# Performance work log

Measured on AMD Instinct MI355X. Metric: run time of the kernel, lower is better.

Reference implementation:

```python
import jax, jax.numpy as jnp
import numpy as np

C, V, B, ITERS = 144, 576, 1024, 3  # checks, variables, batch, decoding iterations
COL_W = 4  # variable-node degree (ones per column of H)


def _make_H():
    """Deterministic sparse 0/1 parity-check matrix, col weight COL_W, row weight >= 2."""
    rng = np.random.default_rng(0)
    H = np.zeros((C, V), np.float32)
    for v in range(V):
        H[rng.choice(C, size=COL_W, replace=False), v] = 1.0
    for c in range(C):
        while H[c].sum() < 2:
            H[c, rng.integers(V)] = 1.0
    return H


def setup_inputs() -> dict:
    key = jax.random.key(0)
    r = jax.random.normal(key, (B, V), dtype=jnp.float32)  # channel LLRs, batched
    alpha = 0.7 * jnp.ones((ITERS,), dtype=jnp.float32)    # nn.Parameter init
    H = jnp.asarray(_make_H())                             # [C, V] 0/1 mask
    return {"r": r, "alpha": alpha, "H": H}


def _c_to_v(M, edge, a):
    """Check-to-variable min-sum messages, vectorized over batch and rows.

    For each edge (c,v): E[c,v] = a * (prod of signs of M[c, edges(c)\\{v}])
                                   * (min of |M[c, edges(c)\\{v}]|)
    Implemented with the standard two-smallest-values trick.
    """
    inf = jnp.float32(jnp.inf)
    absM = jnp.where(edge, jnp.abs(M), inf)                 # [B,C,V]
    min1 = jnp.min(absM, axis=-1, keepdims=True)            # smallest |M| per row
    idx = jnp.argmin(absM, axis=-1)                         # [B,C] its position
    is_min = jnp.arange(V)[None, None, :] == idx[..., None]  # one-hot of argmin
    min2 = jnp.min(jnp.where(is_min, inf, absM), axis=-1, keepdims=True)
    excl_min = jnp.where(is_min, min2, min1)                # min excluding self
    sgn = jnp.where(edge, jnp.sign(M), 1.0)
    row_sign = jnp.prod(sgn, axis=-1, keepdims=True)
    sgn_excl = row_sign * sgn                               # product excluding self (signs are +/-1)
    return jnp.where(edge, a * sgn_excl * excl_min, 0.0)


def reference(r, alpha, H):
    edge = (H == 1.0)[None, :, :]                           # [1,C,V] broadcast to batch
    rB = r[:, None, :]                                      # [B,1,V]
    M = jnp.where(edge, rB, 0.0)                            # initial_M: M[c,v]=r[v] on edges
    E = jnp.zeros_like(M)
    for i in range(alpha.shape[0]):
        E = _c_to_v(M, edge, alpha[i])
        col = jnp.sum(E, axis=1, keepdims=True)             # [B,1,V] sum over checks
        M = jnp.where(edge, col - E + rB, 0.0)              # update_M: extrinsic sum + r[v]
    return r + jnp.sum(E, axis=1)                           # [B,V] output LLRs
```

## Files before the change

kernel.cpp:

```cpp
#include <hip/hip_runtime.h>
#include <stdint.h>

#define CN 144
#define VN 576
#define BN 1024
#define NITER 3
#define RCAP 32
#define NQ   (RCAP/4)
#define CCAP 8
#define TPB 192

#define WS_RLEN 0
#define WS_LOC  192
#define WS_CSC  (192 + CN*VN)
#define WS_CCNT (WS_CSC + CCAP*VN)

__device__ __forceinline__ int edge_id(int l, int c) {
    return (((l >> 2) * CN + c) << 2) | (l & 3);
}

__global__ __launch_bounds__(64) void build_stage(const float* __restrict__ H,
                                                  int* __restrict__ ws) {
    const int c = blockIdx.x;
    const int lane = threadIdx.x;
    int base = 0;
    const float* row = H + c * VN;
    for (int ch = 0; ch < VN / 64; ++ch) {
        const int v = ch * 64 + lane;
        const bool set = row[v] > 0.5f;
        const unsigned long long mask = __ballot(set);
        const int off = base + (int)__popcll(mask & ((1ULL << lane) - 1ULL));
        ws[WS_LOC + v * CN + c] = set ? off : -1;
        base += (int)__popcll(mask);
    }
    if (lane == 0) ws[WS_RLEN + c] = base;
}

__global__ __launch_bounds__(64) void build_csc(int* __restrict__ ws) {
    const int v = blockIdx.x;
    const int lane = threadIdx.x;
    int cnt = 0;
    for (int ch = 0; ch < 3; ++ch) {
        const int c = ch * 64 + lane;
        const int l = (c < CN) ? ws[WS_LOC + v * CN + c] : -1;
        const bool set = (l >= 0) && (l < RCAP);
        const unsigned long long mask = __ballot(set);
        const int off = cnt + (int)__popcll(mask & ((1ULL << lane) - 1ULL));
        if (set && off < CCAP) ws[WS_CSC + off * VN + v] = edge_id(l, c);
        cnt += (int)__popcll(mask);
    }
    if (cnt > CCAP) cnt = CCAP;
    if (lane == 0) ws[WS_CCNT + v] = cnt;
    if (lane >= cnt && lane < CCAP) ws[WS_CSC + lane * VN + v] = 0;
}

__global__ __launch_bounds__(TPB) void ldpc_decode(const float* __restrict__ r,
                                                   const float* __restrict__ alpha,
                                                   const int* __restrict__ ws,
                                                   float* __restrict__ out) {
    __shared__ float4 M4[NQ * CN];
    float* const Mf = reinterpret_cast<float*>(M4);

    const int b = blockIdx.x;
    const int t = threadIdx.x;
    const float a_[NITER] = { alpha[0], alpha[1], alpha[2] };

    int ent4[3][4], entX[3][4];
    int cnt[3];
    float rv[3];
    #pragma unroll
    for (int q = 0; q < 3; ++q) {
        const int v = t + q * TPB;
        rv[q]  = r[b * VN + v];
        cnt[q] = ws[WS_CCNT + v];
        #pragma unroll
        for (int j = 0; j < 4; ++j) ent4[q][j] = ws[WS_CSC + j * VN + v];
    }
    const int rl = (t < CN) ? min(ws[WS_RLEN + t], RCAP) : 0;
    const int any_hi = __syncthreads_or((cnt[0] > 4) | (cnt[1] > 4) | (cnt[2] > 4));
    if (any_hi) {
        #pragma unroll
        for (int q = 0; q < 3; ++q)
            #pragma unroll
            for (int j = 0; j < 4; ++j) entX[q][j] = ws[WS_CSC + (4 + j) * VN + t + q * TPB];
    }

    if (t < CN) {
        const int rpad = (rl + 3) & ~3;
        for (int k = rl; k < rpad; ++k) Mf[edge_id(k, t)] = INFINITY;
    }
    #pragma unroll
    for (int q = 0; q < 3; ++q) {
        #pragma unroll
        for (int j = 0; j < 4; ++j) if (j < cnt[q]) Mf[ent4[q][j]] = rv[q];
    }
    if (any_hi) {
        #pragma unroll
        for (int q = 0; q < 3; ++q) {
            #pragma unroll
            for (int j = 0; j < 4; ++j) if (4 + j < cnt[q]) Mf[entX[q][j]] = rv[q];
        }
    }
    __syncthreads();

    #pragma unroll
    for (int it = 0; it < NITER; ++it) {
        const float a = a_[it];

        if (t < CN) {
            const int nq  = (rl + 3) >> 2;
            const int nqf = rl >> 2;
            float4 mq[NQ];
            uint32_t m1 = 0x7fffffffu, m2 = 0x7fffffffu, sg = 0u;
            #pragma unroll
            for (int q4 = 0; q4 < NQ; ++q4) {
                if (q4 < nq) {
                    mq[q4] = M4[q4 * CN + t];
                    const uint32_t* mu = reinterpret_cast<const uint32_t*>(&mq[q4]);
                    #pragma unroll
                    for (int j = 0; j < 4; ++j) {
                        const uint32_t mb = mu[j];
                        const uint32_t ab = mb & 0x7fffffffu;
                        sg ^= mb;
                        const uint32_t hi = (ab > m1) ? ab : m1;
                        m1 = (ab < m1) ? ab : m1;
                        m2 = (hi < m2) ? hi : m2;
                    }
                }
            }
            sg &= 0x80000000u;
            const uint32_t p1b = __float_as_uint(a * __uint_as_float(m1)) ^ sg;
            const uint32_t p2b = __float_as_uint(a * __uint_as_float(m2)) ^ sg;
            #pragma unroll
            for (int q4 = 0; q4 < NQ; ++q4) {
                if (q4 < nq) {
                    const uint32_t* mu = reinterpret_cast<const uint32_t*>(&mq[q4]);
                    float4 ev;
                    uint32_t* eu = reinterpret_cast<uint32_t*>(&ev);
                    if (q4 < nqf) {
                        #pragma unroll
                        for (int j = 0; j < 4; ++j) {
                            const uint32_t mb = mu[j];
                            const uint32_t ab = mb & 0x7fffffffu;
                            eu[j] = ((ab == m1) ? p2b : p1b) ^ (mb & 0x80000000u);
                        }
                    } else {
                        #pragma unroll
                        for (int j = 0; j < 4; ++j) {
                            const int k = q4 * 4 + j;
                            const uint32_t mb = mu[j];
                            const uint32_t ab = mb & 0x7fffffffu;
                            eu[j] = (k < rl)
                                  ? (((ab == m1) ? p2b : p1b) ^ (mb & 0x80000000u))
                                  : mb;
                        }
                    }
                    M4[q4 * CN + t] = ev;
                }
            }
        }
        __syncthreads();

        #pragma unroll
        for (int q = 0; q < 3; ++q) {
            float E4[4], EX[4];
            float col = 0.0f;
            #pragma unroll
            for (int j = 0; j < 4; ++j) {
                E4[j] = (j < cnt[q]) ? Mf[ent4[q][j]] : 0.0f;
                col += E4[j];
            }
            if (any_hi) {
                #pragma unroll
                for (int j = 0; j < 4; ++j) {
                    EX[j] = (4 + j < cnt[q]) ? Mf[entX[q][j]] : 0.0f;
                    col += EX[j];
                }
            }
            if (it == NITER - 1) {
                out[b * VN + t + q * TPB] = rv[q] + col;
            } else {
                const float mb = col + rv[q];
                #pragma unroll
                for (int j = 0; j < 4; ++j) if (j < cnt[q]) Mf[ent4[q][j]] = mb - E4[j];
                if (any_hi) {
                    #pragma unroll
                    for (int j = 0; j < 4; ++j) if (4 + j < cnt[q]) Mf[entX[q][j]] = mb - EX[j];
                }
            }
        }
        if (it < NITER - 1) __syncthreads();
    }
}

extern "C" void kernel_launch(void* const* d_in, const int* in_sizes, int n_in,
                              void* d_out, int out_size, void* d_ws, size_t ws_size,
                              hipStream_t stream) {
    const float* r     = (const float*)d_in[0];
    const float* alpha = (const float*)d_in[1];
    const float* H     = (const float*)d_in[2];
    float* out = (float*)d_out;
    int* ws    = (int*)d_ws;

    build_stage<<<CN, 64, 0, stream>>>(H, ws);
    build_csc<<<VN, 64, 0, stream>>>(ws);
    ldpc_decode<<<BN, TPB, 0, stream>>>(r, alpha, ws, out);
}
```

Baseline: 23.73 us.

## Fuse graph-building kernels via atomic row-slot counters and fixed-width row scans

The two preprocessing kernels become one. Each column builder now claims a row slot with an atomicAdd on a per-check counter, taken modulo 32, instead of reading a precomputed dense location table. This removes a kernel launch and the large LOC workspace pass. The decoder drops per-row lengths: it pre-fills shared memory with infinities, scans all 8 float4 slots per row, and passes the infinity entries through unchanged. In exchange it does a little more shared-memory and ALU work per iteration, and the counters are never reset between calls, so correctness depends on row degree staying at or below 32.

New measurement: 25.04 us. 1.06x slower.

```diff
diff --git a/kernel.cpp b/kernel.cpp
--- a/kernel.cpp
+++ b/kernel.cpp
@@ -5,48 +5,32 @@
 #define VN 576
 #define BN 1024
 #define NITER 3
-#define RCAP 32
-#define NQ   (RCAP/4)
+#define NQ   8
 #define CCAP 8
 #define TPB 192
 
-#define WS_RLEN 0
-#define WS_LOC  192
-#define WS_CSC  (192 + CN*VN)
-#define WS_CCNT (WS_CSC + CCAP*VN)
+#define WS_RCTR 0
+#define WS_CCNT 144
+#define WS_CSC  720
 
 __device__ __forceinline__ int edge_id(int l, int c) {
     return (((l >> 2) * CN + c) << 2) | (l & 3);
 }
 
-__global__ __launch_bounds__(64) void build_stage(const float* __restrict__ H,
-                                                  int* __restrict__ ws) {
-    const int c = blockIdx.x;
-    const int lane = threadIdx.x;
-    int base = 0;
-    const float* row = H + c * VN;
-    for (int ch = 0; ch < VN / 64; ++ch) {
-        const int v = ch * 64 + lane;
-        const bool set = row[v] > 0.5f;
-        const unsigned long long mask = __ballot(set);
-        const int off = base + (int)__popcll(mask & ((1ULL << lane) - 1ULL));
-        ws[WS_LOC + v * CN + c] = set ? off : -1;
-        base += (int)__popcll(mask);
-    }
-    if (lane == 0) ws[WS_RLEN + c] = base;
-}
-
-__global__ __launch_bounds__(64) void build_csc(int* __restrict__ ws) {
+__global__ __launch_bounds__(64) void build_csc(const float* __restrict__ H,
+                                                int* __restrict__ ws) {
     const int v = blockIdx.x;
     const int lane = threadIdx.x;
     int cnt = 0;
     for (int ch = 0; ch < 3; ++ch) {
         const int c = ch * 64 + lane;
-        const int l = (c < CN) ? ws[WS_LOC + v * CN + c] : -1;
-        const bool set = (l >= 0) && (l < RCAP);
+        const bool set = (c < CN) && (H[c * VN + v] > 0.5f);
         const unsigned long long mask = __ballot(set);
         const int off = cnt + (int)__popcll(mask & ((1ULL << lane) - 1ULL));
-        if (set && off < CCAP) ws[WS_CSC + off * VN + v] = edge_id(l, c);
+        if (set && off < CCAP) {
+            const unsigned old = atomicAdd((unsigned*)(ws + WS_RCTR + c), 1u);
+            ws[WS_CSC + off * VN + v] = edge_id((int)(old & 31u), c);
+        }
         cnt += (int)__popcll(mask);
     }
     if (cnt > CCAP) cnt = CCAP;
@@ -76,7 +60,6 @@
         #pragma unroll
         for (int j = 0; j < 4; ++j) ent4[q][j] = ws[WS_CSC + j * VN + v];
     }
-    const int rl = (t < CN) ? min(ws[WS_RLEN + t], RCAP) : 0;
     const int any_hi = __syncthreads_or((cnt[0] > 4) | (cnt[1] > 4) | (cnt[2] > 4));
     if (any_hi) {
         #pragma unroll
@@ -85,10 +68,9 @@
             for (int j = 0; j < 4; ++j) entX[q][j] = ws[WS_CSC + (4 + j) * VN + t + q * TPB];
     }
 
-    if (t < CN) {
-        const int rpad = (rl + 3) & ~3;
-        for (int k = rl; k < rpad; ++k) Mf[edge_id(k, t)] = INFINITY;
-    }
+    const float4 inf4 = make_float4(INFINITY, INFINITY, INFINITY, INFINITY);
+    for (int i = t; i < NQ * CN; i += TPB) M4[i] = inf4;
+    __syncthreads();
     #pragma unroll
     for (int q = 0; q < 3; ++q) {
         #pragma unroll
@@ -108,24 +90,20 @@
         const float a = a_[it];
 
         if (t < CN) {
-            const int nq  = (rl + 3) >> 2;
-            const int nqf = rl >> 2;
             float4 mq[NQ];
             uint32_t m1 = 0x7fffffffu, m2 = 0x7fffffffu, sg = 0u;
             #pragma unroll
             for (int q4 = 0; q4 < NQ; ++q4) {
-                if (q4 < nq) {
-                    mq[q4] = M4[q4 * CN + t];
-                    const uint32_t* mu = reinterpret_cast<const uint32_t*>(&mq[q4]);
-                    #pragma unroll
-                    for (int j = 0; j < 4; ++j) {
-                        const uint32_t mb = mu[j];
-                        const uint32_t ab = mb & 0x7fffffffu;
-                        sg ^= mb;
-                        const uint32_t hi = (ab > m1) ? ab : m1;
-                        m1 = (ab < m1) ? ab : m1;
-                        m2 = (hi < m2) ? hi : m2;
-                    }
+                mq[q4] = M4[q4 * CN + t];
+                const uint32_t* mu = reinterpret_cast<const uint32_t*>(&mq[q4]);
+                #pragma unroll
+                for (int j = 0; j < 4; ++j) {
+                    const uint32_t mb = mu[j];
+                    const uint32_t ab = mb & 0x7fffffffu;
+                    sg ^= mb;
+                    const uint32_t hi = (ab > m1) ? ab : m1;
+                    m1 = (ab < m1) ? ab : m1;
+                    m2 = (hi < m2) ? hi : m2;
                 }
             }
             sg &= 0x80000000u;
@@ -133,30 +111,17 @@
             const uint32_t p2b = __float_as_uint(a * __uint_as_float(m2)) ^ sg;
             #pragma unroll
             for (int q4 = 0; q4 < NQ; ++q4) {
-                if (q4 < nq) {
-                    const uint32_t* mu = reinterpret_cast<const uint32_t*>(&mq[q4]);
-                    float4 ev;
-                    uint32_t* eu = reinterpret_cast<uint32_t*>(&ev);
-                    if (q4 < nqf) {
-                        #pragma unroll
-                        for (int j = 0; j < 4; ++j) {
-                            const uint32_t mb = mu[j];
-                            const uint32_t ab = mb & 0x7fffffffu;
-                            eu[j] = ((ab == m1) ? p2b : p1b) ^ (mb & 0x80000000u);
-                        }
-                    } else {
-                        #pragma unroll
-                        for (int j = 0; j < 4; ++j) {
-                            const int k = q4 * 4 + j;
-                            const uint32_t mb = mu[j];
-                            const uint32_t ab = mb & 0x7fffffffu;
-                            eu[j] = (k < rl)
-                                  ? (((ab == m1) ? p2b : p1b) ^ (mb & 0x80000000u))
-                                  : mb;
-                        }
-                    }
-                    M4[q4 * CN + t] = ev;
+                const uint32_t* mu = reinterpret_cast<const uint32_t*>(&mq[q4]);
+                float4 ev;
+                uint32_t* eu = reinterpret_cast<uint32_t*>(&ev);
+                #pragma unroll
+                for (int j = 0; j < 4; ++j) {
+                    const uint32_t mb = mu[j];
+                    const uint32_t ab = mb & 0x7fffffffu;
+                    const uint32_t e  = ((ab == m1) ? p2b : p1b) ^ (mb & 0x80000000u);
+                    eu[j] = (ab == 0x7f800000u) ? mb : e;
                 }
+                M4[q4 * CN + t] = ev;
             }
         }
         __syncthreads();
@@ -202,7 +167,6 @@
     float* out = (float*)d_out;
     int* ws    = (int*)d_ws;
 
-    build_stage<<<CN, 64, 0, stream>>>(H, ws);
-    build_csc<<<VN, 64, 0, stream>>>(ws);
+    build_csc<<<VN, 64, 0, stream>>>(H, ws);
     ldpc_decode<<<BN, TPB, 0, stream>>>(r, alpha, ws, out);
 }
```

## Merge two graph-build kernels into one single-block kernel using shared atomics

Applied to the files above, without the earlier changes.

Replaces the two-kernel parity-check graph construction (per-row ballot compaction, then per-column CSC gather through a large global LOC table) with one 1024-thread block. It scans H, assigns row slots and column slots with shared-memory atomics, and writes the row counts, column counts and CSC edge table to the workspace. This removes one kernel launch and the large intermediate global table. In exchange the build runs on a single block scanning all of H serially, and slot order is now nondeterministic, so edge order within a row or column can change. Ordering does not affect the min-sum result except through floating-point summation order.

Measured after the change: 37.58 us. +58.4%, slower.

```diff
diff --git a/kernel.cpp b/kernel.cpp
--- a/kernel.cpp
+++ b/kernel.cpp
@@ -11,47 +11,40 @@
 #define TPB 192
 
 #define WS_RLEN 0
-#define WS_LOC  192
-#define WS_CSC  (192 + CN*VN)
-#define WS_CCNT (WS_CSC + CCAP*VN)
+#define WS_CCNT 144
+#define WS_CSC  720
 
 __device__ __forceinline__ int edge_id(int l, int c) {
     return (((l >> 2) * CN + c) << 2) | (l & 3);
 }
 
-__global__ __launch_bounds__(64) void build_stage(const float* __restrict__ H,
+__global__ __launch_bounds__(1024) void build_one(const float* __restrict__ H,
                                                   int* __restrict__ ws) {
-    const int c = blockIdx.x;
-    const int lane = threadIdx.x;
-    int base = 0;
-    const float* row = H + c * VN;
-    for (int ch = 0; ch < VN / 64; ++ch) {
-        const int v = ch * 64 + lane;
-        const bool set = row[v] > 0.5f;
-        const unsigned long long mask = __ballot(set);
-        const int off = base + (int)__popcll(mask & ((1ULL << lane) - 1ULL));
-        ws[WS_LOC + v * CN + c] = set ? off : -1;
-        base += (int)__popcll(mask);
-    }
-    if (lane == 0) ws[WS_RLEN + c] = base;
-}
-
-__global__ __launch_bounds__(64) void build_csc(int* __restrict__ ws) {
-    const int v = blockIdx.x;
-    const int lane = threadIdx.x;
-    int cnt = 0;
-    for (int ch = 0; ch < 3; ++ch) {
-        const int c = ch * 64 + lane;
-        const int l = (c < CN) ? ws[WS_LOC + v * CN + c] : -1;
-        const bool set = (l >= 0) && (l < RCAP);
-        const unsigned long long mask = __ballot(set);
-        const int off = cnt + (int)__popcll(mask & ((1ULL << lane) - 1ULL));
-        if (set && off < CCAP) ws[WS_CSC + off * VN + v] = edge_id(l, c);
-        cnt += (int)__popcll(mask);
-    }
-    if (cnt > CCAP) cnt = CCAP;
-    if (lane == 0) ws[WS_CCNT + v] = cnt;
-    if (lane >= cnt && lane < CCAP) ws[WS_CSC + lane * VN + v] = 0;
+    __shared__ int rcnt[CN];
+    __shared__ int ccnt[VN];
+    __shared__ int csc[CCAP * VN];
+    const int t = threadIdx.x;
+
+    for (int i = t; i < CN; i += 1024) rcnt[i] = 0;
+    for (int i = t; i < VN; i += 1024) ccnt[i] = 0;
+    for (int i = t; i < CCAP * VN; i += 1024) csc[i] = 0;
+    __syncthreads();
+
+    for (int i = t; i < CN * VN; i += 1024) {
+        if (H[i] > 0.5f) {
+            const int c = i / VN, v = i - c * VN;
+            const int l = atomicAdd(&rcnt[c], 1);
+            if (l < RCAP) {
+                const int pos = atomicAdd(&ccnt[v], 1);
+                if (pos < CCAP) csc[pos * VN + v] = edge_id(l, c);
+            }
+        }
+    }
+    __syncthreads();
+
+    for (int i = t; i < CN; i += 1024) ws[WS_RLEN + i] = rcnt[i];
+    for (int i = t; i < VN; i += 1024) ws[WS_CCNT + i] = min(ccnt[i], CCAP);
+    for (int i = t; i < CCAP * VN; i += 1024) ws[WS_CSC + i] = csc[i];
 }
 
 __global__ __launch_bounds__(TPB) void ldpc_decode(const float* __restrict__ r,
@@ -202,7 +195,6 @@
     float* out = (float*)d_out;
     int* ws    = (int*)d_ws;
 
-    build_stage<<<CN, 64, 0, stream>>>(H, ws);
-    build_csc<<<VN, 64, 0, stream>>>(ws);
+    build_one<<<1, 1024, 0, stream>>>(H, ws);
     ldpc_decode<<<BN, TPB, 0, stream>>>(r, alpha, ws, out);
 }
```

## Shrink decode block to a single wave with nine variables per thread

Applied to the files above, without the earlier changes.

Reduces the decoder block from 192 to 64 threads. Each thread now handles nine variable nodes and up to three check rows. The block-wide OR reduction becomes a wavefront __any. This aims to cut cross-wave barrier cost and allow more independent blocks per CU. In exchange it triples per-thread serial work, raises register pressure from larger index arrays, and leaves part of the wave idle on the last check row.

New measurement: 35.92 us. +51.4%, slower.

```diff
diff --git a/kernel.cpp b/kernel.cpp
--- a/kernel.cpp
+++ b/kernel.cpp
@@ -8,7 +8,8 @@
 #define RCAP 32
 #define NQ   (RCAP/4)
 #define CCAP 8
-#define TPB 192
+#define TPB 64
+#define CPT 9
 
 #define WS_RLEN 0
 #define WS_LOC  192
@@ -65,40 +66,53 @@
     const int t = threadIdx.x;
     const float a_[NITER] = { alpha[0], alpha[1], alpha[2] };
 
-    int ent4[3][4], entX[3][4];
-    int cnt[3];
-    float rv[3];
-    #pragma unroll
-    for (int q = 0; q < 3; ++q) {
-        const int v = t + q * TPB;
-        rv[q]  = r[b * VN + v];
-        cnt[q] = ws[WS_CCNT + v];
-        #pragma unroll
-        for (int j = 0; j < 4; ++j) ent4[q][j] = ws[WS_CSC + j * VN + v];
-    }
-    const int rl = (t < CN) ? min(ws[WS_RLEN + t], RCAP) : 0;
-    const int any_hi = __syncthreads_or((cnt[0] > 4) | (cnt[1] > 4) | (cnt[2] > 4));
+    int   ent4[CPT][4], entX[CPT][4];
+    int   cnt[CPT];
+    float rv[CPT];
+    #pragma unroll
+    for (int k = 0; k < CPT; ++k) {
+        const int v = t + k * 64;
+        rv[k]  = r[b * VN + v];
+        cnt[k] = ws[WS_CCNT + v];
+        #pragma unroll
+        for (int j = 0; j < 4; ++j) ent4[k][j] = ws[WS_CSC + j * VN + v];
+    }
+    bool hi = false;
+    #pragma unroll
+    for (int k = 0; k < CPT; ++k) hi |= (cnt[k] > 4);
+    const bool any_hi = __any(hi);
     if (any_hi) {
         #pragma unroll
-        for (int q = 0; q < 3; ++q)
+        for (int k = 0; k < CPT; ++k)
             #pragma unroll
-            for (int j = 0; j < 4; ++j) entX[q][j] = ws[WS_CSC + (4 + j) * VN + t + q * TPB];
-    }
-
-    if (t < CN) {
-        const int rpad = (rl + 3) & ~3;
-        for (int k = rl; k < rpad; ++k) Mf[edge_id(k, t)] = INFINITY;
-    }
-    #pragma unroll
-    for (int q = 0; q < 3; ++q) {
-        #pragma unroll
-        for (int j = 0; j < 4; ++j) if (j < cnt[q]) Mf[ent4[q][j]] = rv[q];
+            for (int j = 0; j < 4; ++j) entX[k][j] = ws[WS_CSC + (4 + j) * VN + t + k * 64];
+    }
+
+    int rl[3];
+    #pragma unroll
+    for (int cr = 0; cr < 3; ++cr) {
+        const int c = t + cr * 64;
+        rl[cr] = (c < CN) ? min(ws[WS_RLEN + c], RCAP) : 0;
+    }
+
+    #pragma unroll
+    for (int cr = 0; cr < 3; ++cr) {
+        const int c = t + cr * 64;
+        if (c < CN) {
+            const int rpad = (rl[cr] + 3) & ~3;
+            for (int k = rl[cr]; k < rpad; ++k) Mf[edge_id(k, c)] = INFINITY;
+        }
+    }
+    #pragma unroll
+    for (int k = 0; k < CPT; ++k) {
+        #pragma unroll
+        for (int j = 0; j < 4; ++j) if (j < cnt[k]) Mf[ent4[k][j]] = rv[k];
     }
     if (any_hi) {
         #pragma unroll
-        for (int q = 0; q < 3; ++q) {
+        for (int k = 0; k < CPT; ++k) {
             #pragma unroll
-            for (int j = 0; j < 4; ++j) if (4 + j < cnt[q]) Mf[entX[q][j]] = rv[q];
+            for (int j = 0; j < 4; ++j) if (4 + j < cnt[k]) Mf[entX[k][j]] = rv[k];
         }
     }
     __syncthreads();
@@ -107,85 +121,90 @@
     for (int it = 0; it < NITER; ++it) {
         const float a = a_[it];
 
-        if (t < CN) {
-            const int nq  = (rl + 3) >> 2;
-            const int nqf = rl >> 2;
-            float4 mq[NQ];
-            uint32_t m1 = 0x7fffffffu, m2 = 0x7fffffffu, sg = 0u;
-            #pragma unroll
-            for (int q4 = 0; q4 < NQ; ++q4) {
-                if (q4 < nq) {
-                    mq[q4] = M4[q4 * CN + t];
-                    const uint32_t* mu = reinterpret_cast<const uint32_t*>(&mq[q4]);
-                    #pragma unroll
-                    for (int j = 0; j < 4; ++j) {
-                        const uint32_t mb = mu[j];
-                        const uint32_t ab = mb & 0x7fffffffu;
-                        sg ^= mb;
-                        const uint32_t hi = (ab > m1) ? ab : m1;
-                        m1 = (ab < m1) ? ab : m1;
-                        m2 = (hi < m2) ? hi : m2;
-                    }
-                }
-            }
-            sg &= 0x80000000u;
-            const uint32_t p1b = __float_as_uint(a * __uint_as_float(m1)) ^ sg;
-            const uint32_t p2b = __float_as_uint(a * __uint_as_float(m2)) ^ sg;
-            #pragma unroll
-            for (int q4 = 0; q4 < NQ; ++q4) {
-                if (q4 < nq) {
-                    const uint32_t* mu = reinterpret_cast<const uint32_t*>(&mq[q4]);
-                    float4 ev;
-                    uint32_t* eu = reinterpret_cast<uint32_t*>(&ev);
-                    if (q4 < nqf) {
+        #pragma unroll
+        for (int cr = 0; cr < 3; ++cr) {
+            const int c = t + cr * 64;
+            if (c < CN) {
+                const int rlc = rl[cr];
+                const int nq  = (rlc + 3) >> 2;
+                const int nqf = rlc >> 2;
+                float4 mq[NQ];
+                uint32_t m1 = 0x7fffffffu, m2 = 0x7fffffffu, sg = 0u;
+                #pragma unroll
+                for (int q4 = 0; q4 < NQ; ++q4) {
+                    if (q4 < nq) {
+                        mq[q4] = M4[q4 * CN + c];
+                        const uint32_t* mu = reinterpret_cast<const uint32_t*>(&mq[q4]);
                         #pragma unroll
                         for (int j = 0; j < 4; ++j) {
                             const uint32_t mb = mu[j];
                             const uint32_t ab = mb & 0x7fffffffu;
-                            eu[j] = ((ab == m1) ? p2b : p1b) ^ (mb & 0x80000000u);
-                        }
-                    } else {
-                        #pragma unroll
-                        for (int j = 0; j < 4; ++j) {
-                            const int k = q4 * 4 + j;
-                            const uint32_t mb = mu[j];
-                            const uint32_t ab = mb & 0x7fffffffu;
-                            eu[j] = (k < rl)
-                                  ? (((ab == m1) ? p2b : p1b) ^ (mb & 0x80000000u))
-                                  : mb;
+                            sg ^= mb;
+                            const uint32_t hi2 = (ab > m1) ? ab : m1;
+                            m1 = (ab < m1) ? ab : m1;
+                            m2 = (hi2 < m2) ? hi2 : m2;
                         }
                     }
-                    M4[q4 * CN + t] = ev;
+                }
+                sg &= 0x80000000u;
+                const uint32_t p1b = __float_as_uint(a * __uint_as_float(m1)) ^ sg;
+                const uint32_t p2b = __float_as_uint(a * __uint_as_float(m2)) ^ sg;
+                #pragma unroll
+                for (int q4 = 0; q4 < NQ; ++q4) {
+                    if (q4 < nq) {
+                        const uint32_t* mu = reinterpret_cast<const uint32_t*>(&mq[q4]);
+                        float4 ev;
+                        uint32_t* eu = reinterpret_cast<uint32_t*>(&ev);
+                        if (q4 < nqf) {
+                            #pragma unroll
+                            for (int j = 0; j < 4; ++j) {
+                                const uint32_t mb = mu[j];
+                                const uint32_t ab = mb & 0x7fffffffu;
+                                eu[j] = ((ab == m1) ? p2b : p1b) ^ (mb & 0x80000000u);
+                            }
+                        } else {
+                            #pragma unroll
+                            for (int j = 0; j < 4; ++j) {
+                                const int k = q4 * 4 + j;
+                                const uint32_t mb = mu[j];
+                                const uint32_t ab = mb & 0x7fffffffu;
+                                eu[j] = (k < rlc)
+                                      ? (((ab == m1) ? p2b : p1b) ^ (mb & 0x80000000u))
+                                      : mb;
+                            }
+                        }
+                        M4[q4 * CN + c] = ev;
+                    }
                 }
             }
         }
         __syncthreads();
 
         #pragma unroll
-        for (int q = 0; q < 3; ++q) {
+        for (int k = 0; k < CPT; ++k) {
             float E4[4], EX[4];
             float col = 0.0f;
             #pragma unroll
             for (int j = 0; j < 4; ++j) {
-                E4[j] = (j < cnt[q]) ? Mf[ent4[q][j]] : 0.0f;
+                E4[j] = (j < cnt[k]) ? Mf[ent4[k][j]] : 0.0f;
                 col += E4[j];
             }
             if (any_hi) {
                 #pragma unroll
                 for (int j = 0; j < 4; ++j) {
-                    EX[j] = (4 + j < cnt[q]) ? Mf[entX[q][j]] : 0.0f;
+                    EX[j] = (4 + j < cnt[k]) ? Mf[entX[k][j]] : 0.0f;
                     col += EX[j];
                 }
             }
             if (it == NITER - 1) {
-                out[b * VN + t + q * TPB] = rv[q] + col;
+                out[b * VN + t + k * 64] = rv[k] + col;
             } else {
-                const float mb = col + rv[q];
-                #pragma unroll
-                for (int j = 0; j < 4; ++j) if (j < cnt[q]) Mf[ent4[q][j]] = mb - E4[j];
+                const float mb = col + rv[k];
+                #pragma unroll
+                for (int j = 0; j < 4; ++j) if (j < cnt[k]) Mf[ent4[k][j]] = mb - E4[j];
                 if (any_hi) {
                     #pragma unroll
-                    for (int j = 0; j < 4; ++j) if (4 + j < cnt[q]) Mf[entX[q][j]] = mb - EX[j];
+                    for (int j = 0; j < 4; ++j) if (4 + j < cnt[k]) Mf[entX[k][j]] = mb - EX[j];
                 }
             }
         }
```
